# Kernel tuning notes

Measured on AMD Instinct MI355X. Metric: run time of the kernel, lower is better.

## Reference

```python
import jax, jax.numpy as jnp
import numpy as np

D_MODEL = 1024
N_HEADS = 16
HEAD_DIM = D_MODEL // N_HEADS
WINDOW = 256
NEG_INF = -1e30  # finite stand-in for -inf; identical softmax result, NaN-safe


def setup_inputs() -> dict:
    key = jax.random.key(0)
    ks = jax.random.split(key, 5)
    B, L = 1, 4096
    s = 1.0 / np.sqrt(D_MODEL)
    return {
        "x": jax.random.normal(ks[0], (B, L, D_MODEL), dtype=jnp.float32),
        "Wq": jax.random.normal(ks[1], (D_MODEL, D_MODEL), dtype=jnp.float32) * s,
        "Wk": jax.random.normal(ks[2], (D_MODEL, D_MODEL), dtype=jnp.float32) * s,
        "Wv": jax.random.normal(ks[3], (D_MODEL, D_MODEL), dtype=jnp.float32) * s,
        "Wo": jax.random.normal(ks[4], (D_MODEL, D_MODEL), dtype=jnp.float32) * s,
    }


def reference(x, Wq, Wk, Wv, Wo):
    B, L, _ = x.shape
    # projections (nn.Linear applies x @ W.T; weights here are stored as [out,in])
    q = (x @ Wq.T).reshape(B, L, N_HEADS, HEAD_DIM).transpose(0, 2, 1, 3)  # [B,H,L,Dh]
    k = (x @ Wk.T).reshape(B, L, N_HEADS, HEAD_DIM).transpose(0, 2, 1, 3)
    v = (x @ Wv.T).reshape(B, L, N_HEADS, HEAD_DIM).transpose(0, 2, 1, 3)

    # sliding-window causal mask: position i attends to j in [i-WINDOW+1, i]
    i = jnp.arange(L)[:, None]
    j = jnp.arange(L)[None, :]
    allowed = (j <= i) & (j >= i - WINDOW + 1)  # [L,L] bool

    scale = 1.0 / jnp.sqrt(jnp.asarray(HEAD_DIM, dtype=q.dtype))
    scores = jnp.einsum("bhqd,bhkd->bhqk", q, k) * scale  # [B,H,L,L]
    scores = jnp.where(allowed, scores, NEG_INF)
    attn = jax.nn.softmax(scores, axis=-1)
    out = jnp.einsum("bhqk,bhkd->bhqd", attn, v)  # [B,H,L,Dh]
    out = out.transpose(0, 2, 1, 3).reshape(B, L, D_MODEL)
    return out @ Wo.T
```

## Files before the change

### kernel.cpp

```cpp
#include <hip/hip_runtime.h>

using bf16x8 = __attribute__((ext_vector_type(8))) short;
using u16x8  = __attribute__((ext_vector_type(8))) unsigned short;
using f32x4  = __attribute__((ext_vector_type(4))) float;

#define LSEQ   4096
#define NH     16
#define DH     64
#define WIN    256
#define DM     1024

__device__ __forceinline__ void gl2lds16(const void* g, void* l) {
  __builtin_amdgcn_global_load_lds(
      (const __attribute__((address_space(1))) unsigned int*)g,
      (__attribute__((address_space(3))) unsigned int*)l,
      16, 0, 0);
}

__device__ __forceinline__ unsigned short f2bf(float f) {
  unsigned int u = __float_as_uint(f);
  u += 0x7fffu + ((u >> 16) & 1u);
  return (unsigned short)(u >> 16);
}

__global__ __launch_bounds__(256) void cvt_all(
    const float* __restrict__ x,  const float* __restrict__ wq,
    const float* __restrict__ wk, const float* __restrict__ wv,
    const float* __restrict__ wo, unsigned short* __restrict__ dst)
{
  const size_t i = ((size_t)blockIdx.x * 256 + threadIdx.x) * 8;
  const size_t XN = (size_t)LSEQ * DM;
  const float* src;
  size_t off;
  if (i < XN) { src = x; off = i; }
  else {
    const size_t j = i - XN;
    const int s = (int)(j >> 20);
    off = j & ((1u << 20) - 1);
    src = (s == 0) ? wq : (s == 1) ? wk : (s == 2) ? wv : wo;
  }
  const f32x4 f0 = *(const f32x4*)(src + off);
  const f32x4 f1 = *(const f32x4*)(src + off + 4);
  u16x8 o;
  o[0] = f2bf(f0[0]); o[1] = f2bf(f0[1]); o[2] = f2bf(f0[2]); o[3] = f2bf(f0[3]);
  o[4] = f2bf(f1[0]); o[5] = f2bf(f1[1]); o[6] = f2bf(f1[2]); o[7] = f2bf(f1[3]);
  *(u16x8*)(dst + i) = o;
}

__device__ __forceinline__ void gemm_tile_db(
    const unsigned short* __restrict__ X,
    const unsigned short* __restrict__ W,
    int m0, int n0,
    unsigned short* As0, unsigned short* Bs0,
    f32x4 (&acc)[4][4])
{
  const int tid  = threadIdx.x;
  const int lane = tid & 63;
  const int wave = tid >> 6;
  const int wm = wave >> 1, wn = wave & 1;
  const int fr = lane & 15, quad = lane >> 4;
  const int sw = fr & 7;

  const f32x4 zero = {0.f, 0.f, 0.f, 0.f};
  #pragma unroll
  for (int i = 0; i < 4; ++i)
    #pragma unroll
    for (int j = 0; j < 4; ++j)
      acc[i][j] = zero;

  const unsigned short* ga[4];
  const unsigned short* gb[4];
  int lc[4];
  #pragma unroll
  for (int cc = 0; cc < 4; ++cc) {
    const int c = tid + cc * 256;
    const int row = c >> 3;
    const int gp  = (c & 7) ^ (row & 7);
    ga[cc] = X + (size_t)(m0 + row) * DM + gp * 8;
    gb[cc] = W + (size_t)(n0 + row) * DM + gp * 8;
    lc[cc] = c * 16;
  }
  char* laA = (char*)As0;
  char* laB = (char*)Bs0;

  #pragma unroll
  for (int cc = 0; cc < 4; ++cc) {
    gl2lds16(ga[cc], laA + lc[cc]);
    gl2lds16(gb[cc], laB + lc[cc]);
  }
  __syncthreads();

  #define PITER(KT, CUR, NXT)                                                 \
    do {                                                                      \
      if ((KT) + 64 < DM) {                                                   \
        _Pragma("unroll")                                                     \
        for (int cc = 0; cc < 4; ++cc) {                                      \
          gl2lds16(ga[cc] + (KT) + 64, laA + (NXT) * 16384 + lc[cc]);         \
          gl2lds16(gb[cc] + (KT) + 64, laB + (NXT) * 16384 + lc[cc]);         \
        }                                                                     \
      }                                                                       \
      const unsigned short* As_ = As0 + (CUR) * 8192;                         \
      const unsigned short* Bs_ = Bs0 + (CUR) * 8192;                         \
      _Pragma("unroll")                                                       \
      for (int s = 0; s < 2; ++s) {                                           \
        bf16x8 a[4], b[4];                                                    \
        _Pragma("unroll")                                                     \
        for (int t = 0; t < 4; ++t)                                           \
          a[t] = *(const bf16x8*)(As_ + (wm * 64 + t * 16 + fr) * 64          \
                                      + (((s * 4 + quad) ^ sw) * 8));         \
        _Pragma("unroll")                                                     \
        for (int t = 0; t < 4; ++t)                                           \
          b[t] = *(const bf16x8*)(Bs_ + (wn * 64 + t * 16 + fr) * 64          \
                                      + (((s * 4 + quad) ^ sw) * 8));         \
        __builtin_amdgcn_s_setprio(1);                                        \
        _Pragma("unroll")                                                     \
        for (int i = 0; i < 4; ++i)                                           \
          _Pragma("unroll")                                                   \
          for (int j = 0; j < 4; ++j)                                         \
            acc[i][j] = __builtin_amdgcn_mfma_f32_16x16x32_bf16(              \
                a[i], b[j], acc[i][j], 0, 0, 0);                              \
        __builtin_amdgcn_s_setprio(0);                                        \
      }                                                                       \
      __syncthreads();                                                        \
    } while (0)

  #pragma unroll 1
  for (int kt2 = 0; kt2 < DM; kt2 += 128) {
    PITER(kt2,      0, 1);
    PITER(kt2 + 64, 1, 0);
  }
  #undef PITER
}

__global__ __launch_bounds__(256) void proj_gemm(
    const unsigned short* __restrict__ X,
    const unsigned short* __restrict__ Wq,
    const unsigned short* __restrict__ Wk,
    const unsigned short* __restrict__ Wv,
    unsigned short* __restrict__ Qo,
    unsigned short* __restrict__ Ko,
    unsigned short* __restrict__ Vt)
{
  __shared__ __align__(16) unsigned short As[2 * 128 * 64];
  __shared__ __align__(16) unsigned short Bs[2 * 128 * 64];
  const int id = blockIdx.x;
  const int lane = threadIdx.x & 63;
  const int wave = threadIdx.x >> 6;
  const int wm = wave >> 1, wn = wave & 1;
  const int cn = lane & 15, quad = lane >> 4;
  f32x4 acc[4][4];

  if (id < 512) {
    const int m0   = (id & 31) * 128;
    const int by   = id >> 5;
    const int wsel = by >> 3;
    const int n0   = (by & 7) * 128;
    gemm_tile_db(X, wsel ? Wk : Wq, m0, n0, As, Bs, acc);

    const float qscl = wsel ? 1.0f : 0.180336881f;
    unsigned short* O = wsel ? Ko : Qo;
    #pragma unroll
    for (int i = 0; i < 4; ++i)
      #pragma unroll
      for (int j = 0; j < 4; ++j)
        #pragma unroll
        for (int r = 0; r < 4; ++r) {
          const int row = m0 + wm * 64 + i * 16 + quad * 4 + r;
          const int col = n0 + wn * 64 + j * 16 + cn;
          const int h = col >> 6, d = col & 63;
          O[(size_t)(h * LSEQ + row) * DH + d] = f2bf(acc[i][j][r] * qscl);
        }
  } else {
    const int vid = id - 512;
    const int m0 = (vid & 7) * 128;
    const int n0 = (vid >> 3) * 128;
    gemm_tile_db(Wv, X, m0, n0, As, Bs, acc);

    #pragma unroll
    for (int i = 0; i < 4; ++i)
      #pragma unroll
      for (int j = 0; j < 4; ++j)
        #pragma unroll
        for (int r = 0; r < 4; ++r) {
          const int row = m0 + wm * 64 + i * 16 + quad * 4 + r;
          const int col = n0 + wn * 64 + j * 16 + cn;
          Vt[(size_t)row * LSEQ + col] = f2bf(acc[i][j][r]);
        }
  }
}

__global__ __launch_bounds__(256) void out_gemm(
    const unsigned short* __restrict__ X,
    const unsigned short* __restrict__ W,
    float* __restrict__ O)
{
  __shared__ unsigned short As2[64 * 64];
  __shared__ unsigned short Bs[128 * 64];
  const int m0 = blockIdx.x * 64;
  const int n0 = blockIdx.y * 128;
  const int tid  = threadIdx.x;
  const int lane = tid & 63;
  const int wave = tid >> 6;
  const int wm = wave >> 1, wn = wave & 1;
  const int fr = lane & 15, quad = lane >> 4;

  const f32x4 zero = {0.f, 0.f, 0.f, 0.f};
  f32x4 acc[2][4];
  #pragma unroll
  for (int i = 0; i < 2; ++i)
    #pragma unroll
    for (int j = 0; j < 4; ++j)
      acc[i][j] = zero;

  const unsigned short* ga[2];
  char* la[2];
  #pragma unroll
  for (int cc = 0; cc < 2; ++cc) {
    const int c = tid + cc * 256;
    const int row = c >> 3;
    const int gpp = (c & 7) ^ (row & 7);
    ga[cc] = X + (size_t)(m0 + row) * DM + gpp * 8;
    la[cc] = (char*)As2 + c * 16;
  }
  const unsigned short* gb[4];
  char* lb[4];
  #pragma unroll
  for (int cc = 0; cc < 4; ++cc) {
    const int c = tid + cc * 256;
    const int row = c >> 3;
    const int gpp = (c & 7) ^ (row & 7);
    gb[cc] = W + (size_t)(n0 + row) * DM + gpp * 8;
    lb[cc] = (char*)Bs + c * 16;
  }

  const int sw = fr & 7;
  for (int kt = 0; kt < DM; kt += 64) {
    #pragma unroll
    for (int cc = 0; cc < 2; ++cc)
      gl2lds16(ga[cc] + kt, la[cc]);
    #pragma unroll
    for (int cc = 0; cc < 4; ++cc)
      gl2lds16(gb[cc] + kt, lb[cc]);
    __syncthreads();

    #pragma unroll
    for (int s = 0; s < 2; ++s) {
      bf16x8 a[2], b[4];
      #pragma unroll
      for (int t = 0; t < 2; ++t)
        a[t] = *(const bf16x8*)(As2 + (wm * 32 + t * 16 + fr) * 64
                                    + (((s * 4 + quad) ^ sw) * 8));
      #pragma unroll
      for (int t = 0; t < 4; ++t)
        b[t] = *(const bf16x8*)(Bs + (wn * 64 + t * 16 + fr) * 64
                                   + (((s * 4 + quad) ^ sw) * 8));
      #pragma unroll
      for (int i = 0; i < 2; ++i)
        #pragma unroll
        for (int j = 0; j < 4; ++j)
          acc[i][j] = __builtin_amdgcn_mfma_f32_16x16x32_bf16(a[i], b[j], acc[i][j], 0, 0, 0);
    }
    __syncthreads();
  }

  const int cn = lane & 15;
  #pragma unroll
  for (int i = 0; i < 2; ++i)
    #pragma unroll
    for (int j = 0; j < 4; ++j)
      #pragma unroll
      for (int r = 0; r < 4; ++r) {
        const int row = m0 + wm * 32 + i * 16 + quad * 4 + r;
        const int col = n0 + wn * 64 + j * 16 + cn;
        O[(size_t)row * DM + col] = acc[i][j][r];
      }
}

#define PSTR 72
__global__ __launch_bounds__(512) void attn_fwd(
    const unsigned short* __restrict__ Q,
    const unsigned short* __restrict__ K,
    const unsigned short* __restrict__ Vt,
    unsigned short* __restrict__ Oa)
{
  __shared__ unsigned short Ks[2][64 * PSTR];
  __shared__ unsigned short Vs[2][64 * PSTR];
  __shared__ unsigned short Pl[8][16 * PSTR];
  const int id   = blockIdx.x;
  const int h    = (id & 7) | ((id >> 8) << 3);
  const int bq0  = ((id >> 3) & 31) * 128;
  const int tid  = threadIdx.x;
  const int wave = tid >> 6;
  const int lane = tid & 63;
  const int n = lane & 15, quad = lane >> 4;
  const int q0 = bq0 + wave * 16;
  unsigned short* pl = Pl[wave];

  const size_t qbase = ((size_t)(h * LSEQ + q0 + n)) * DH + quad * 8;
  const bf16x8 aq0 = *(const bf16x8*)(Q + qbase);
  const bf16x8 aq1 = *(const bf16x8*)(Q + qbase + 32);

  const int lo = (bq0 >= WIN) ? (bq0 - WIN) : 0;
  const int hi = bq0 + 128;

  const int krow = tid >> 3, part = tid & 7;
  const size_t kg = ((size_t)(h * LSEQ + krow)) * DH + part * 8;
  const size_t vg = ((size_t)(h * DH + krow)) * LSEQ + part * 8;
  const int ld = krow * PSTR + part * 8;

  {
    *(bf16x8*)(Ks[0] + ld) = *(const bf16x8*)(K  + kg + (size_t)lo * DH);
    *(bf16x8*)(Vs[0] + ld) = *(const bf16x8*)(Vt + vg + lo);
  }
  __syncthreads();

  const f32x4 zero = {0.f, 0.f, 0.f, 0.f};
  f32x4 acc[4] = {zero, zero, zero, zero};
  float li[4] = {0.f, 0.f, 0.f, 0.f};

  int t = 0;
  for (int jb = lo; jb < hi; jb += 64, ++t) {
    const int buf = t & 1;
    const bool more = (jb + 64 < hi);
    bf16x8 nk, nv;
    if (more) {
      nk = *(const bf16x8*)(K  + kg + (size_t)(jb + 64) * DH);
      nv = *(const bf16x8*)(Vt + vg + (jb + 64));
    }
    const bool active = (jb <= q0 + 15) && (jb + 63 >= q0 - (WIN - 1));
    if (active) {
      const unsigned short* ks = Ks[buf];
      const unsigned short* vs = Vs[buf];
      f32x4 s[4];
      __builtin_amdgcn_s_setprio(1);
      #pragma unroll
      for (int u = 0; u < 4; ++u) {
        const bf16x8 kb0 = *(const bf16x8*)(ks + (u * 16 + n) * PSTR + quad * 8);
        const bf16x8 kb1 = *(const bf16x8*)(ks + (u * 16 + n) * PSTR + 32 + quad * 8);
        f32x4 c = zero;
        c = __builtin_amdgcn_mfma_f32_16x16x32_bf16(aq0, kb0, c, 0, 0, 0);
        c = __builtin_amdgcn_mfma_f32_16x16x32_bf16(aq1, kb1, c, 0, 0, 0);
        s[u] = c;
      }
      __builtin_amdgcn_s_setprio(0);
      const bool nomask = (jb + 63 <= q0) && (jb >= q0 + 15 - (WIN - 1));
      if (nomask) {
        #pragma unroll
        for (int u = 0; u < 4; ++u)
          #pragma unroll
          for (int r = 0; r < 4; ++r) {
            const float e = __builtin_exp2f(s[u][r] - 32.0f);
            s[u][r] = e;
            li[r] += e;
          }
      } else {
        #pragma unroll
        for (int u = 0; u < 4; ++u)
          #pragma unroll
          for (int r = 0; r < 4; ++r) {
            const int qi = q0 + quad * 4 + r;
            const int kj = jb + u * 16 + n;
            const bool ok = (kj <= qi) && (kj + WIN > qi);
            const float e = __builtin_exp2f(ok ? s[u][r] - 32.0f : -1e30f);
            s[u][r] = e;
            li[r] += e;
          }
      }
      #pragma unroll
      for (int u = 0; u < 4; ++u)
        #pragma unroll
        for (int r = 0; r < 4; ++r)
          pl[(quad * 4 + r) * PSTR + u * 16 + n] = f2bf(s[u][r]);
      asm volatile("s_waitcnt lgkmcnt(0)" ::: "memory");
      const bf16x8 pa0 = *(const bf16x8*)(pl + n * PSTR + quad * 8);
      const bf16x8 pa1 = *(const bf16x8*)(pl + n * PSTR + 32 + quad * 8);
      __builtin_amdgcn_s_setprio(1);
      #pragma unroll
      for (int ct = 0; ct < 4; ++ct) {
        const bf16x8 vb0 = *(const bf16x8*)(vs + (ct * 16 + n) * PSTR + quad * 8);
        const bf16x8 vb1 = *(const bf16x8*)(vs + (ct * 16 + n) * PSTR + 32 + quad * 8);
        acc[ct] = __builtin_amdgcn_mfma_f32_16x16x32_bf16(pa0, vb0, acc[ct], 0, 0, 0);
        acc[ct] = __builtin_amdgcn_mfma_f32_16x16x32_bf16(pa1, vb1, acc[ct], 0, 0, 0);
      }
      __builtin_amdgcn_s_setprio(0);
    }
    if (more) {
      *(bf16x8*)(Ks[buf ^ 1] + ld) = nk;
      *(bf16x8*)(Vs[buf ^ 1] + ld) = nv;
    }
    __syncthreads();
  }

  float rd[4];
  #pragma unroll
  for (int r = 0; r < 4; ++r) {
    float v = li[r];
    v += __shfl_xor(v, 1);
    v += __shfl_xor(v, 2);
    v += __shfl_xor(v, 4);
    v += __shfl_xor(v, 8);
    rd[r] = 1.0f / v;
  }
  #pragma unroll
  for (int ct = 0; ct < 4; ++ct)
    #pragma unroll
    for (int r = 0; r < 4; ++r) {
      const int row = q0 + quad * 4 + r;
      const int col = h * DH + ct * 16 + n;
      Oa[(size_t)row * DM + col] = f2bf(acc[ct][r] * rd[r]);
    }
}

extern "C" void kernel_launch(void* const* d_in, const int* in_sizes, int n_in,
                              void* d_out, int out_size, void* d_ws, size_t ws_size,
                              hipStream_t stream) {
  const float* x  = (const float*)d_in[0];
  const float* Wq = (const float*)d_in[1];
  const float* Wk = (const float*)d_in[2];
  const float* Wv = (const float*)d_in[3];
  const float* Wo = (const float*)d_in[4];
  float* out = (float*)d_out;

  unsigned short* xb  = (unsigned short*)d_ws;
  unsigned short* Wqb = xb  + (size_t)LSEQ * DM;
  unsigned short* Wkb = Wqb + (size_t)DM * DM;
  unsigned short* Wvb = Wkb + (size_t)DM * DM;
  unsigned short* Wob = Wvb + (size_t)DM * DM;
  unsigned short* Q    = Wob + (size_t)DM * DM;
  unsigned short* K    = Q   + (size_t)LSEQ * DM;
  unsigned short* Vt   = K   + (size_t)LSEQ * DM;
  unsigned short* Attn = Vt  + (size_t)LSEQ * DM;

  cvt_all<<<dim3(4096), 256, 0, stream>>>(x, Wq, Wk, Wv, Wo, xb);
  proj_gemm<<<dim3(768), 256, 0, stream>>>(xb, Wqb, Wkb, Wvb, Q, K, Vt);
  attn_fwd<<<dim3(512), 512, 0, stream>>>(Q, K, Vt, Attn);
  out_gemm<<<dim3(64, 8), 256, 0, stream>>>(Attn, Wob, out);
}
```

Before: 152.8 us.

## Use 8-wave projection GEMM blocks and double-buffer the output GEMM

The projection GEMM now launches 512 threads per block. Each of the 8 waves owns a 64x32 sub-tile instead of 4 waves owning 64x64, which halves per-wave accumulators and global-to-LDS loads per thread. The output GEMM moves from a single LDS buffer with two barriers per k-step to a double-buffered prefetch loop with MFMA priority boosts. This is meant to overlap loads with compute. The cost is doubled LDS use and fewer MFMAs per fragment load in the projection.

```diff
diff --git a/kernel.cpp b/kernel.cpp
--- a/kernel.cpp
+++ b/kernel.cpp
@@ -47,17 +47,18 @@
   *(u16x8*)(dst + i) = o;
 }
 
-__device__ __forceinline__ void gemm_tile_db(
+__device__ __forceinline__ void gemm_tile_db8(
     const unsigned short* __restrict__ X,
     const unsigned short* __restrict__ W,
     int m0, int n0,
     unsigned short* As0, unsigned short* Bs0,
-    f32x4 (&acc)[4][4])
+    f32x4 (&acc)[4][2])
 {
   const int tid  = threadIdx.x;
   const int lane = tid & 63;
   const int wave = tid >> 6;
-  const int wm = wave >> 1, wn = wave & 1;
+  const int wm = wave >> 2;
+  const int wn = wave & 3;
   const int fr = lane & 15, quad = lane >> 4;
   const int sw = fr & 7;
 
@@ -65,15 +66,15 @@
   #pragma unroll
   for (int i = 0; i < 4; ++i)
     #pragma unroll
-    for (int j = 0; j < 4; ++j)
+    for (int j = 0; j < 2; ++j)
       acc[i][j] = zero;
 
-  const unsigned short* ga[4];
-  const unsigned short* gb[4];
-  int lc[4];
-  #pragma unroll
-  for (int cc = 0; cc < 4; ++cc) {
-    const int c = tid + cc * 256;
+  const unsigned short* ga[2];
+  const unsigned short* gb[2];
+  int lc[2];
+  #pragma unroll
+  for (int cc = 0; cc < 2; ++cc) {
+    const int c = tid + cc * 512;
     const int row = c >> 3;
     const int gp  = (c & 7) ^ (row & 7);
     ga[cc] = X + (size_t)(m0 + row) * DM + gp * 8;
@@ -84,7 +85,7 @@
   char* laB = (char*)Bs0;
 
   #pragma unroll
-  for (int cc = 0; cc < 4; ++cc) {
+  for (int cc = 0; cc < 2; ++cc) {
     gl2lds16(ga[cc], laA + lc[cc]);
     gl2lds16(gb[cc], laB + lc[cc]);
   }
@@ -94,7 +95,7 @@
     do {                                                                      \
       if ((KT) + 64 < DM) {                                                   \
         _Pragma("unroll")                                                     \
-        for (int cc = 0; cc < 4; ++cc) {                                      \
+        for (int cc = 0; cc < 2; ++cc) {                                      \
           gl2lds16(ga[cc] + (KT) + 64, laA + (NXT) * 16384 + lc[cc]);         \
           gl2lds16(gb[cc] + (KT) + 64, laB + (NXT) * 16384 + lc[cc]);         \
         }                                                                     \
@@ -103,20 +104,20 @@
       const unsigned short* Bs_ = Bs0 + (CUR) * 8192;                         \
       _Pragma("unroll")                                                       \
       for (int s = 0; s < 2; ++s) {                                           \
-        bf16x8 a[4], b[4];                                                    \
+        bf16x8 a[4], b[2];                                                    \
         _Pragma("unroll")                                                     \
         for (int t = 0; t < 4; ++t)                                           \
           a[t] = *(const bf16x8*)(As_ + (wm * 64 + t * 16 + fr) * 64          \
                                       + (((s * 4 + quad) ^ sw) * 8));         \
         _Pragma("unroll")                                                     \
-        for (int t = 0; t < 4; ++t)                                           \
-          b[t] = *(const bf16x8*)(Bs_ + (wn * 64 + t * 16 + fr) * 64          \
+        for (int t = 0; t < 2; ++t)                                           \
+          b[t] = *(const bf16x8*)(Bs_ + (wn * 32 + t * 16 + fr) * 64          \
                                       + (((s * 4 + quad) ^ sw) * 8));         \
         __builtin_amdgcn_s_setprio(1);                                        \
         _Pragma("unroll")                                                     \
         for (int i = 0; i < 4; ++i)                                           \
           _Pragma("unroll")                                                   \
-          for (int j = 0; j < 4; ++j)                                         \
+          for (int j = 0; j < 2; ++j)                                         \
             acc[i][j] = __builtin_amdgcn_mfma_f32_16x16x32_bf16(              \
                 a[i], b[j], acc[i][j], 0, 0, 0);                              \
         __builtin_amdgcn_s_setprio(0);                                        \
@@ -132,7 +133,7 @@
   #undef PITER
 }
 
-__global__ __launch_bounds__(256) void proj_gemm(
+__global__ __launch_bounds__(512) void proj_gemm(
     const unsigned short* __restrict__ X,
     const unsigned short* __restrict__ Wq,
     const unsigned short* __restrict__ Wk,
@@ -146,27 +147,27 @@
   const int id = blockIdx.x;
   const int lane = threadIdx.x & 63;
   const int wave = threadIdx.x >> 6;
-  const int wm = wave >> 1, wn = wave & 1;
+  const int wm = wave >> 2, wn = wave & 3;
   const int cn = lane & 15, quad = lane >> 4;
-  f32x4 acc[4][4];
+  f32x4 acc[4][2];
 
   if (id < 512) {
     const int m0   = (id & 31) * 128;
     const int by   = id >> 5;
     const int wsel = by >> 3;
     const int n0   = (by & 7) * 128;
-    gemm_tile_db(X, wsel ? Wk : Wq, m0, n0, As, Bs, acc);
+    gemm_tile_db8(X, wsel ? Wk : Wq, m0, n0, As, Bs, acc);
 
     const float qscl = wsel ? 1.0f : 0.180336881f;
     unsigned short* O = wsel ? Ko : Qo;
     #pragma unroll
     for (int i = 0; i < 4; ++i)
       #pragma unroll
-      for (int j = 0; j < 4; ++j)
+      for (int j = 0; j < 2; ++j)
         #pragma unroll
         for (int r = 0; r < 4; ++r) {
           const int row = m0 + wm * 64 + i * 16 + quad * 4 + r;
-          const int col = n0 + wn * 64 + j * 16 + cn;
+          const int col = n0 + wn * 32 + j * 16 + cn;
           const int h = col >> 6, d = col & 63;
           O[(size_t)(h * LSEQ + row) * DH + d] = f2bf(acc[i][j][r] * qscl);
         }
@@ -174,16 +175,16 @@
     const int vid = id - 512;
     const int m0 = (vid & 7) * 128;
     const int n0 = (vid >> 3) * 128;
-    gemm_tile_db(Wv, X, m0, n0, As, Bs, acc);
+    gemm_tile_db8(Wv, X, m0, n0, As, Bs, acc);
 
     #pragma unroll
     for (int i = 0; i < 4; ++i)
       #pragma unroll
-      for (int j = 0; j < 4; ++j)
+      for (int j = 0; j < 2; ++j)
         #pragma unroll
         for (int r = 0; r < 4; ++r) {
           const int row = m0 + wm * 64 + i * 16 + quad * 4 + r;
-          const int col = n0 + wn * 64 + j * 16 + cn;
+          const int col = n0 + wn * 32 + j * 16 + cn;
           Vt[(size_t)row * LSEQ + col] = f2bf(acc[i][j][r]);
         }
   }
@@ -194,8 +195,8 @@
     const unsigned short* __restrict__ W,
     float* __restrict__ O)
 {
-  __shared__ unsigned short As2[64 * 64];
-  __shared__ unsigned short Bs[128 * 64];
+  __shared__ __align__(16) unsigned short As2[2 * 64 * 64];
+  __shared__ __align__(16) unsigned short Bs[2 * 128 * 64];
   const int m0 = blockIdx.x * 64;
   const int n0 = blockIdx.y * 128;
   const int tid  = threadIdx.x;
@@ -203,6 +204,7 @@
   const int wave = tid >> 6;
   const int wm = wave >> 1, wn = wave & 1;
   const int fr = lane & 15, quad = lane >> 4;
+  const int sw = fr & 7;
 
   const f32x4 zero = {0.f, 0.f, 0.f, 0.f};
   f32x4 acc[2][4];
@@ -213,55 +215,75 @@
       acc[i][j] = zero;
 
   const unsigned short* ga[2];
-  char* la[2];
+  int lca[2];
   #pragma unroll
   for (int cc = 0; cc < 2; ++cc) {
     const int c = tid + cc * 256;
     const int row = c >> 3;
     const int gpp = (c & 7) ^ (row & 7);
     ga[cc] = X + (size_t)(m0 + row) * DM + gpp * 8;
-    la[cc] = (char*)As2 + c * 16;
+    lca[cc] = c * 16;
   }
   const unsigned short* gb[4];
-  char* lb[4];
+  int lcb[4];
   #pragma unroll
   for (int cc = 0; cc < 4; ++cc) {
     const int c = tid + cc * 256;
     const int row = c >> 3;
     const int gpp = (c & 7) ^ (row & 7);
     gb[cc] = W + (size_t)(n0 + row) * DM + gpp * 8;
-    lb[cc] = (char*)Bs + c * 16;
-  }
-
-  const int sw = fr & 7;
-  for (int kt = 0; kt < DM; kt += 64) {
-    #pragma unroll
-    for (int cc = 0; cc < 2; ++cc)
-      gl2lds16(ga[cc] + kt, la[cc]);
-    #pragma unroll
-    for (int cc = 0; cc < 4; ++cc)
-      gl2lds16(gb[cc] + kt, lb[cc]);
-    __syncthreads();
-
-    #pragma unroll
-    for (int s = 0; s < 2; ++s) {
-      bf16x8 a[2], b[4];
-      #pragma unroll
-      for (int t = 0; t < 2; ++t)
-        a[t] = *(const bf16x8*)(As2 + (wm * 32 + t * 16 + fr) * 64
-                                    + (((s * 4 + quad) ^ sw) * 8));
-      #pragma unroll
-      for (int t = 0; t < 4; ++t)
-        b[t] = *(const bf16x8*)(Bs + (wn * 64 + t * 16 + fr) * 64
-                                   + (((s * 4 + quad) ^ sw) * 8));
-      #pragma unroll
-      for (int i = 0; i < 2; ++i)
-        #pragma unroll
-        for (int j = 0; j < 4; ++j)
-          acc[i][j] = __builtin_amdgcn_mfma_f32_16x16x32_bf16(a[i], b[j], acc[i][j], 0, 0, 0);
-    }
-    __syncthreads();
-  }
+    lcb[cc] = c * 16;
+  }
+  char* laA = (char*)As2;
+  char* laB = (char*)Bs;
+
+  #pragma unroll
+  for (int cc = 0; cc < 2; ++cc) gl2lds16(ga[cc], laA + lca[cc]);
+  #pragma unroll
+  for (int cc = 0; cc < 4; ++cc) gl2lds16(gb[cc], laB + lcb[cc]);
+  __syncthreads();
+
+  #define OITER(KT, CUR, NXT)                                                 \
+    do {                                                                      \
+      if ((KT) + 64 < DM) {                                                   \
+        _Pragma("unroll")                                                     \
+        for (int cc = 0; cc < 2; ++cc)                                        \
+          gl2lds16(ga[cc] + (KT) + 64, laA + (NXT) * 8192 + lca[cc]);         \
+        _Pragma("unroll")                                                     \
+        for (int cc = 0; cc < 4; ++cc)                                        \
+          gl2lds16(gb[cc] + (KT) + 64, laB + (NXT) * 16384 + lcb[cc]);        \
+      }                                                                       \
+      const unsigned short* As_ = As2 + (CUR) * 4096;                         \
+      const unsigned short* Bs_ = Bs + (CUR) * 8192;                          \
+      _Pragma("unroll")                                                       \
+      for (int s = 0; s < 2; ++s) {                                           \
+        bf16x8 a[2], b[4];                                                    \
+        _Pragma("unroll")                                                     \
+        for (int t = 0; t < 2; ++t)                                           \
+          a[t] = *(const bf16x8*)(As_ + (wm * 32 + t * 16 + fr) * 64          \
+                                      + (((s * 4 + quad) ^ sw) * 8));         \
+        _Pragma("unroll")                                                     \
+        for (int t = 0; t < 4; ++t)                                           \
+          b[t] = *(const bf16x8*)(Bs_ + (wn * 64 + t * 16 + fr) * 64          \
+                                      + (((s * 4 + quad) ^ sw) * 8));         \
+        __builtin_amdgcn_s_setprio(1);                                        \
+        _Pragma("unroll")                                                     \
+        for (int i = 0; i < 2; ++i)                                           \
+          _Pragma("unroll")                                                   \
+          for (int j = 0; j < 4; ++j)                                         \
+            acc[i][j] = __builtin_amdgcn_mfma_f32_16x16x32_bf16(              \
+                a[i], b[j], acc[i][j], 0, 0, 0);                              \
+        __builtin_amdgcn_s_setprio(0);                                        \
+      }                                                                       \
+      __syncthreads();                                                        \
+    } while (0)
+
+  #pragma unroll 1
+  for (int kt2 = 0; kt2 < DM; kt2 += 128) {
+    OITER(kt2,      0, 1);
+    OITER(kt2 + 64, 1, 0);
+  }
+  #undef OITER
 
   const int cn = lane & 15;
   #pragma unroll
@@ -432,7 +454,7 @@
   unsigned short* Attn = Vt  + (size_t)LSEQ * DM;
 
   cvt_all<<<dim3(4096), 256, 0, stream>>>(x, Wq, Wk, Wv, Wo, xb);
-  proj_gemm<<<dim3(768), 256, 0, stream>>>(xb, Wqb, Wkb, Wvb, Q, K, Vt);
+  proj_gemm<<<dim3(768), 512, 0, stream>>>(xb, Wqb, Wkb, Wvb, Q, K, Vt);
   attn_fwd<<<dim3(512), 512, 0, stream>>>(Q, K, Vt, Attn);
   out_gemm<<<dim3(64, 8), 256, 0, stream>>>(Attn, Wob, out);
 }
```

New measurement: 152.4 us, median of 2. About the same (-0.2%).
